# Performance work log

Measured on AMD Instinct MI355X. Metric: run time of the kernel, lower is better.

Reference implementation:

```python
import jax, jax.numpy as jnp
import numpy as np

NUM_EXPERTS = 8
IN_FEATURES = 1024
HIDDEN_FEATURES = 4096
OUT_FEATURES = 1024
TOKENS = 8192


def setup_inputs() -> dict:
    key = jax.random.key(0)
    k_x, k_idx, k_w1, k_w2, k_b1, k_b2 = jax.random.split(key, 6)
    x = jax.random.normal(k_x, (TOKENS, IN_FEATURES), dtype=jnp.float32)
    indices_s = jax.random.randint(k_idx, (TOKENS,), 0, NUM_EXPERTS, dtype=jnp.int64)
    # learned parameters (torch uses torch.rand; scaled for numeric sanity)
    weight1 = jax.random.normal(k_w1, (NUM_EXPERTS, IN_FEATURES, HIDDEN_FEATURES), dtype=jnp.float32) * 0.02
    weight2 = jax.random.normal(k_w2, (NUM_EXPERTS, HIDDEN_FEATURES, OUT_FEATURES), dtype=jnp.float32) * 0.02
    bias1 = jax.random.normal(k_b1, (NUM_EXPERTS, HIDDEN_FEATURES), dtype=jnp.float32) * 0.02
    bias2 = jax.random.normal(k_b2, (NUM_EXPERTS, IN_FEATURES), dtype=jnp.float32) * 0.02
    return {"x": x, "indices_s": indices_s, "weight1": weight1, "weight2": weight2, "bias1": bias1, "bias2": bias2}


def reference(x, indices_s, weight1, weight2, bias1, bias2):
    # Per-token expert MLP. Rather than gathering full weight matrices per
    # token (weight[indices_s] -> [T, in, hid], huge), loop over the small
    # fixed expert set and mask-combine. Math identical to the torch module.
    T = x.shape[0]
    num_experts = weight1.shape[0]
    out = jnp.zeros((T, weight2.shape[2]), dtype=x.dtype)
    for e in range(num_experts):
        mask = (indices_s == e)[:, None]  # [T, 1]
        h = jax.nn.gelu(x @ weight1[e] + bias1[e], approximate=False)  # [T, hid]
        y = h @ weight2[e] + bias2[e]  # [T, out]
        out = out + jnp.where(mask, y, jnp.zeros((), dtype=x.dtype))
    # original returns shape [T, 1, out] (x was unsqueezed)
    return out[:, None, :]
```

## Files before the change

kernel.cpp:

```cpp
#include <hip/hip_runtime.h>
#include <hip/hip_bf16.h>
#include <math.h>

#define TOKENS 8192
#define IN_F   1024
#define HID_F  4096
#define OUT_F  1024
#define NEXP   8
#define TSLOTS 72

typedef __attribute__((ext_vector_type(8))) short bf16x8;
typedef __attribute__((ext_vector_type(4))) float f32x4;
typedef __attribute__((ext_vector_type(8))) unsigned short u16x8;

__device__ __forceinline__ unsigned short f2bf(float f) {
    unsigned int u = __float_as_uint(f);
    u += 0x7fffu + ((u >> 16) & 1u);
    return (unsigned short)(u >> 16);
}

__device__ __forceinline__ void gload_lds16(const unsigned short* g, unsigned char* lds) {
    __builtin_amdgcn_global_load_lds(
        (const __attribute__((address_space(1))) void*)g,
        (__attribute__((address_space(3))) void*)lds, 16, 0, 0);
}

__global__ void sort_kernel(const int* __restrict__ idx, int* __restrict__ perm,
                            int* __restrict__ off, int* __restrict__ table) {
    __shared__ int cnt[NEXP];
    __shared__ int base[NEXP];
    const int tid = threadIdx.x, lane = tid & 63;
    if (tid < NEXP) cnt[tid] = 0;
    __syncthreads();
    for (int i = tid; i < TOKENS; i += 1024) {
        int e = idx[i];
#pragma unroll
        for (int ex = 0; ex < NEXP; ++ex) {
            unsigned long long m = __ballot(e == ex);
            if (lane == 0 && m) atomicAdd(&cnt[ex], __popcll(m));
        }
    }
    __syncthreads();
    if (tid == 0) {
        int s = 0;
        for (int e = 0; e < NEXP; ++e) { off[e] = s; base[e] = s; s += cnt[e]; }
        off[NEXP] = s;
        int t = 0;
        for (int e = 0; e < NEXP; ++e)
            for (int m0 = off[e]; m0 < off[e + 1]; m0 += 128)
                table[t++] = (e << 13) | m0;
        for (; t < TSLOTS; ++t) table[t] = -1;
    }
    __syncthreads();
    for (int i = tid; i < TOKENS; i += 1024) {
        int e = idx[i];
#pragma unroll
        for (int ex = 0; ex < NEXP; ++ex) {
            unsigned long long m = __ballot(e == ex);
            if (e == ex) {
                int lead = (int)__ffsll((long long)m) - 1;
                int pos = 0;
                if (lane == lead) pos = atomicAdd(&base[ex], __popcll(m));
                pos = __shfl(pos, lead);
                pos += __popcll(m & ((1ULL << lane) - 1ULL));
                perm[pos] = i;
            }
        }
    }
}

__global__ void gather_x(const float* __restrict__ x, const int* __restrict__ perm,
                         unsigned short* __restrict__ xg) {
    const int row = blockIdx.x, t = threadIdx.x;
    const int src = perm[row];
    float4 v = *(const float4*)(x + (size_t)src * IN_F + t * 4);
    unsigned long long pk =
        (unsigned long long)f2bf(v.x) |
        ((unsigned long long)f2bf(v.y) << 16) |
        ((unsigned long long)f2bf(v.z) << 32) |
        ((unsigned long long)f2bf(v.w) << 48);
    *(unsigned long long*)(xg + (size_t)row * IN_F + t * 4) = pk;
}

__global__ void transp(const float* __restrict__ in, unsigned short* __restrict__ out,
                       int R, int C) {
    __shared__ unsigned short T[64 * 65];
    const int e = blockIdx.z;
    const int r0 = blockIdx.y * 64, c0 = blockIdx.x * 64;
    const int tid = threadIdx.x;
    const int rr = tid >> 4, cc = tid & 15;
    const float* ip = in + ((size_t)e * R + r0) * C + c0;
#pragma unroll
    for (int p = 0; p < 4; ++p) {
        int r = p * 16 + rr;
        float4 v = *(const float4*)(ip + (size_t)r * C + cc * 4);
        T[(cc * 4 + 0) * 65 + r] = f2bf(v.x);
        T[(cc * 4 + 1) * 65 + r] = f2bf(v.y);
        T[(cc * 4 + 2) * 65 + r] = f2bf(v.z);
        T[(cc * 4 + 3) * 65 + r] = f2bf(v.w);
    }
    __syncthreads();
    unsigned short* op = out + ((size_t)e * C + c0) * R + r0;
    const int c = tid >> 2, ch = tid & 3;
    u16x8 a, b;
#pragma unroll
    for (int i = 0; i < 8; ++i) a[i] = T[c * 65 + ch * 16 + i];
#pragma unroll
    for (int i = 0; i < 8; ++i) b[i] = T[c * 65 + ch * 16 + 8 + i];
    *(u16x8*)(op + (size_t)c * R + ch * 16) = a;
    *(u16x8*)(op + (size_t)c * R + ch * 16 + 8) = b;
}

template<int K, int ND, bool GELU>
__launch_bounds__(256, 2)
__global__ void moe_gemm(const unsigned short* __restrict__ A,
                         const unsigned short* __restrict__ W,
                         const float* __restrict__ bias,
                         const int* __restrict__ perm,
                         const int* __restrict__ off,
                         const int* __restrict__ table,
                         void* __restrict__ outp) {
    const int nwg = (ND / 128) * TSLOTS;
    const int chunk = nwg >> 3;
    const int bid = blockIdx.x;
    const int logical = (bid & 7) * chunk + (bid >> 3);
    const int nt = logical / TSLOTS;
    const int t  = logical - nt * TSLOTS;
    const int te = table[t];
    if (te < 0) return;
    const int e  = te >> 13;
    const int m0 = te & 8191;
    const int sege = off[e + 1];
    const int n0 = nt * 128;

    __shared__ __align__(16) unsigned char As[16384];
    __shared__ __align__(16) unsigned char Bs[16384];

    const int tid = threadIdx.x;
    const int wid = tid >> 6, lane = tid & 63;
    const int wm = (wid >> 1) * 64, wn = (wid & 1) * 64;
    const int lr = lane & 15, hk = lane >> 4;

    const unsigned short* We = W + (size_t)e * ND * K + (size_t)n0 * K;

    const int srow   = lane >> 3;
    const int schunk = (lane & 7) ^ srow;

    f32x4 acc[4][4];
#pragma unroll
    for (int i = 0; i < 4; ++i)
#pragma unroll
        for (int j = 0; j < 4; ++j) acc[i][j] = (f32x4){0.f, 0.f, 0.f, 0.f};

    for (int k0 = 0; k0 < K; k0 += 64) {
        __syncthreads();
#pragma unroll
        for (int j = 0; j < 4; ++j) {
            int rt = (wid * 4 + j) * 8 + srow;
            int ga = m0 + rt; if (ga > TOKENS - 1) ga = TOKENS - 1;
            gload_lds16(A  + (size_t)ga * K + k0 + schunk * 8, As + (wid * 4 + j) * 1024);
            gload_lds16(We + (size_t)rt * K + k0 + schunk * 8, Bs + (wid * 4 + j) * 1024);
        }
        __syncthreads();
#pragma unroll
        for (int kk = 0; kk < 2; ++kk) {
            bf16x8 a[4], b[4];
#pragma unroll
            for (int m = 0; m < 4; ++m) {
                int row = wm + m * 16 + lr;
                a[m] = *(const bf16x8*)(As + row * 128 + (((kk * 4 + hk) ^ (lr & 7)) * 16));
            }
#pragma unroll
            for (int n = 0; n < 4; ++n) {
                int row = wn + n * 16 + lr;
                b[n] = *(const bf16x8*)(Bs + row * 128 + (((kk * 4 + hk) ^ (lr & 7)) * 16));
            }
#pragma unroll
            for (int m = 0; m < 4; ++m)
#pragma unroll
                for (int n = 0; n < 4; ++n)
                    acc[m][n] = __builtin_amdgcn_mfma_f32_16x16x32_bf16(a[m], b[n], acc[m][n], 0, 0, 0);
        }
    }

    const float* be = bias + (size_t)e * ND + n0;
#pragma unroll
    for (int m = 0; m < 4; ++m) {
#pragma unroll
        for (int r = 0; r < 4; ++r) {
            int row = wm + m * 16 + hk * 4 + r;
            int grow = m0 + row;
            if (grow >= sege) continue;
            if constexpr (GELU) {
                unsigned short* h = (unsigned short*)outp;
                size_t base = (size_t)grow * ND + n0;
#pragma unroll
                for (int n = 0; n < 4; ++n) {
                    int col = wn + n * 16 + lr;
                    float v = acc[m][n][r] + be[col];
                    float u = v * (0.7978845608f + 0.0356774081f * v * v);
                    float g = v / (1.0f + __expf(-2.0f * u));
                    h[base + col] = f2bf(g);
                }
            } else {
                float* out = (float*)outp;
                int tok = perm[grow];
                size_t base = (size_t)tok * ND + n0;
#pragma unroll
                for (int n = 0; n < 4; ++n) {
                    int col = wn + n * 16 + lr;
                    out[base + col] = acc[m][n][r] + be[col];
                }
            }
        }
    }
}

extern "C" void kernel_launch(void* const* d_in, const int* in_sizes, int n_in,
                              void* d_out, int out_size, void* d_ws, size_t ws_size,
                              hipStream_t stream) {
    const float* x   = (const float*)d_in[0];
    const int*   idx = (const int*)d_in[1];
    const float* w1  = (const float*)d_in[2];
    const float* w2  = (const float*)d_in[3];
    const float* b1  = (const float*)d_in[4];
    const float* b2  = (const float*)d_in[5];
    float* out = (float*)d_out;

    int* perm  = (int*)d_ws;
    int* off   = perm + TOKENS;
    int* table = off + 16;
    unsigned short* xg = (unsigned short*)((char*)d_ws + 65536);
    unsigned short* h  = xg + (size_t)TOKENS * IN_F;
    unsigned short* wt = h + (size_t)TOKENS * HID_F;

    hipLaunchKernelGGL(sort_kernel, dim3(1), dim3(1024), 0, stream, idx, perm, off, table);
    hipLaunchKernelGGL(gather_x, dim3(TOKENS), dim3(256), 0, stream, x, perm, xg);

    hipLaunchKernelGGL(transp, dim3(HID_F / 64, IN_F / 64, NEXP), dim3(256), 0, stream,
                       w1, wt, IN_F, HID_F);
    hipLaunchKernelGGL((moe_gemm<IN_F, HID_F, true>), dim3((HID_F / 128) * TSLOTS), dim3(256),
                       0, stream, xg, wt, b1, perm, off, table, (void*)h);

    hipLaunchKernelGGL(transp, dim3(OUT_F / 64, HID_F / 64, NEXP), dim3(256), 0, stream,
                       w2, wt, HID_F, OUT_F);
    hipLaunchKernelGGL((moe_gemm<HID_F, OUT_F, false>), dim3((OUT_F / 128) * TSLOTS), dim3(256),
                       0, stream, h, wt, b2, perm, off, table, (void*)out);
}
```

Measured before the change: 351.1 us.

## Pipeline MoE GEMM with 4-stage LDS ring buffer and async global loads

Replaces the single-buffered k-loop (two barriers per 64-wide k step) with a 4-deep ring of 32-wide k stages in 64 KB of LDS. Loads are issued three stages ahead and gated with explicit vmcnt waits, so there is one barrier per stage. The LDS swizzle changes to suit the 64-byte rows, and the MFMA block is raised in priority with setprio. The goal is to hide global-to-LDS load latency behind compute, at the cost of 64 KB of LDS per block, which may limit occupancy to 2 blocks per CU or below.

```diff
diff --git a/kernel.cpp b/kernel.cpp
--- a/kernel.cpp
+++ b/kernel.cpp
@@ -113,13 +113,13 @@
 
 template<int K, int ND, bool GELU>
 __launch_bounds__(256, 2)
-__global__ void moe_gemm(const unsigned short* __restrict__ A,
-                         const unsigned short* __restrict__ W,
-                         const float* __restrict__ bias,
-                         const int* __restrict__ perm,
-                         const int* __restrict__ off,
-                         const int* __restrict__ table,
-                         void* __restrict__ outp) {
+__global__ void moe_gemm_pipe(const unsigned short* __restrict__ A,
+                              const unsigned short* __restrict__ W,
+                              const float* __restrict__ bias,
+                              const int* __restrict__ perm,
+                              const int* __restrict__ off,
+                              const int* __restrict__ table,
+                              void* __restrict__ outp) {
     const int nwg = (ND / 128) * TSLOTS;
     const int chunk = nwg >> 3;
     const int bid = blockIdx.x;
@@ -133,8 +133,7 @@
     const int sege = off[e + 1];
     const int n0 = nt * 128;
 
-    __shared__ __align__(16) unsigned char As[16384];
-    __shared__ __align__(16) unsigned char Bs[16384];
+    __shared__ __align__(16) unsigned char L[65536];
 
     const int tid = threadIdx.x;
     const int wid = tid >> 6, lane = tid & 63;
@@ -143,8 +142,27 @@
 
     const unsigned short* We = W + (size_t)e * ND * K + (size_t)n0 * K;
 
-    const int srow   = lane >> 3;
-    const int schunk = (lane & 7) ^ srow;
+    const int id0 = tid, id1 = tid + 256;
+    const int ar0 = id0 >> 2, ac0 = (id0 & 3) ^ ((ar0 >> 1) & 3);
+    const int ar1 = id1 >> 2, ac1 = (id1 & 3) ^ ((ar1 >> 1) & 3);
+    int ga0 = m0 + ar0; if (ga0 > TOKENS - 1) ga0 = TOKENS - 1;
+    int ga1 = m0 + ar1; if (ga1 > TOKENS - 1) ga1 = TOKENS - 1;
+    const unsigned short* sA0 = A + (size_t)ga0 * K + ac0 * 8;
+    const unsigned short* sA1 = A + (size_t)ga1 * K + ac1 * 8;
+    const unsigned short* sB0 = We + (size_t)ar0 * K + ac0 * 8;
+    const unsigned short* sB1 = We + (size_t)ar1 * K + ac1 * 8;
+    const int du = wid * 1024;
+
+    constexpr int NS = K / 32;
+
+    auto stage = [&](int s) {
+        unsigned char* base = L + (s & 3) * 16384;
+        const int ko = s * 32;
+        gload_lds16(sA0 + ko, base + du);
+        gload_lds16(sA1 + ko, base + 4096 + du);
+        gload_lds16(sB0 + ko, base + 8192 + du);
+        gload_lds16(sB1 + ko, base + 12288 + du);
+    };
 
     f32x4 acc[4][4];
 #pragma unroll
@@ -152,35 +170,36 @@
 #pragma unroll
         for (int j = 0; j < 4; ++j) acc[i][j] = (f32x4){0.f, 0.f, 0.f, 0.f};
 
-    for (int k0 = 0; k0 < K; k0 += 64) {
-        __syncthreads();
-#pragma unroll
-        for (int j = 0; j < 4; ++j) {
-            int rt = (wid * 4 + j) * 8 + srow;
-            int ga = m0 + rt; if (ga > TOKENS - 1) ga = TOKENS - 1;
-            gload_lds16(A  + (size_t)ga * K + k0 + schunk * 8, As + (wid * 4 + j) * 1024);
-            gload_lds16(We + (size_t)rt * K + k0 + schunk * 8, Bs + (wid * 4 + j) * 1024);
-        }
-        __syncthreads();
-#pragma unroll
-        for (int kk = 0; kk < 2; ++kk) {
-            bf16x8 a[4], b[4];
-#pragma unroll
-            for (int m = 0; m < 4; ++m) {
-                int row = wm + m * 16 + lr;
-                a[m] = *(const bf16x8*)(As + row * 128 + (((kk * 4 + hk) ^ (lr & 7)) * 16));
-            }
-#pragma unroll
-            for (int n = 0; n < 4; ++n) {
-                int row = wn + n * 16 + lr;
-                b[n] = *(const bf16x8*)(Bs + row * 128 + (((kk * 4 + hk) ^ (lr & 7)) * 16));
-            }
-#pragma unroll
-            for (int m = 0; m < 4; ++m)
-#pragma unroll
-                for (int n = 0; n < 4; ++n)
-                    acc[m][n] = __builtin_amdgcn_mfma_f32_16x16x32_bf16(a[m], b[n], acc[m][n], 0, 0, 0);
-        }
+    stage(0); stage(1); stage(2);
+
+    for (int s = 0; s < NS; ++s) {
+        const int rem = NS - 1 - s;
+        if (rem >= 2)      asm volatile("s_waitcnt vmcnt(8)" ::: "memory");
+        else if (rem == 1) asm volatile("s_waitcnt vmcnt(4)" ::: "memory");
+        else               asm volatile("s_waitcnt vmcnt(0)" ::: "memory");
+        __builtin_amdgcn_s_barrier();
+        __builtin_amdgcn_sched_barrier(0);
+        if (s + 3 < NS) stage(s + 3);
+
+        const unsigned char* base = L + (s & 3) * 16384;
+        bf16x8 a[4], b[4];
+#pragma unroll
+        for (int m = 0; m < 4; ++m) {
+            int row = wm + m * 16 + lr;
+            a[m] = *(const bf16x8*)(base + row * 64 + ((hk ^ ((row >> 1) & 3)) << 4));
+        }
+#pragma unroll
+        for (int n = 0; n < 4; ++n) {
+            int row = wn + n * 16 + lr;
+            b[n] = *(const bf16x8*)(base + 8192 + row * 64 + ((hk ^ ((row >> 1) & 3)) << 4));
+        }
+        __builtin_amdgcn_s_setprio(1);
+#pragma unroll
+        for (int m = 0; m < 4; ++m)
+#pragma unroll
+            for (int n = 0; n < 4; ++n)
+                acc[m][n] = __builtin_amdgcn_mfma_f32_16x16x32_bf16(a[m], b[n], acc[m][n], 0, 0, 0);
+        __builtin_amdgcn_s_setprio(0);
     }
 
     const float* be = bias + (size_t)e * ND + n0;
@@ -239,11 +258,11 @@
 
     hipLaunchKernelGGL(transp, dim3(HID_F / 64, IN_F / 64, NEXP), dim3(256), 0, stream,
                        w1, wt, IN_F, HID_F);
-    hipLaunchKernelGGL((moe_gemm<IN_F, HID_F, true>), dim3((HID_F / 128) * TSLOTS), dim3(256),
+    hipLaunchKernelGGL((moe_gemm_pipe<IN_F, HID_F, true>), dim3((HID_F / 128) * TSLOTS), dim3(256),
                        0, stream, xg, wt, b1, perm, off, table, (void*)h);
 
     hipLaunchKernelGGL(transp, dim3(OUT_F / 64, HID_F / 64, NEXP), dim3(256), 0, stream,
                        w2, wt, HID_F, OUT_F);
-    hipLaunchKernelGGL((moe_gemm<HID_F, OUT_F, false>), dim3((OUT_F / 128) * TSLOTS), dim3(256),
+    hipLaunchKernelGGL((moe_gemm_pipe<HID_F, OUT_F, false>), dim3((OUT_F / 128) * TSLOTS), dim3(256),
                        0, stream, h, wt, b2, perm, off, table, (void*)out);
 }
```

Result: slower. 367.6 us (+4.7%).

## Use 256x256 MoE GEMM tiles with double-buffered LDS and interleaved prefetch

Applied to the files above, without the earlier changes.

Replaces the 128x128, 256-thread grouped GEMM with a 256x256 tile kernel using 512 threads and 128KB of double-buffered LDS. Token slots are now 256 rows, so TSLOTS drops to 40. The next K-tile is staged in four pieces interleaved with MFMA blocks, and s_setprio is raised around the MFMA bursts to overlap loads with compute. This increases operand reuse per LDS load and cuts global traffic. In exchange it gives far fewer workgroups, notably only 160 for the second GEMM on a 256-CU part, and higher register pressure.

```diff
diff --git a/kernel.cpp b/kernel.cpp
--- a/kernel.cpp
+++ b/kernel.cpp
@@ -7,7 +7,7 @@
 #define HID_F  4096
 #define OUT_F  1024
 #define NEXP   8
-#define TSLOTS 72
+#define TSLOTS 40
 
 typedef __attribute__((ext_vector_type(8))) short bf16x8;
 typedef __attribute__((ext_vector_type(4))) float f32x4;
@@ -47,7 +47,7 @@
         off[NEXP] = s;
         int t = 0;
         for (int e = 0; e < NEXP; ++e)
-            for (int m0 = off[e]; m0 < off[e + 1]; m0 += 128)
+            for (int m0 = off[e]; m0 < off[e + 1]; m0 += 256)
                 table[t++] = (e << 13) | m0;
         for (; t < TSLOTS; ++t) table[t] = -1;
     }
@@ -112,83 +112,141 @@
 }
 
 template<int K, int ND, bool GELU>
-__launch_bounds__(256, 2)
-__global__ void moe_gemm(const unsigned short* __restrict__ A,
-                         const unsigned short* __restrict__ W,
-                         const float* __restrict__ bias,
-                         const int* __restrict__ perm,
-                         const int* __restrict__ off,
-                         const int* __restrict__ table,
-                         void* __restrict__ outp) {
-    const int nwg = (ND / 128) * TSLOTS;
+__launch_bounds__(512, 2)
+__global__ void moe_gemm256(const unsigned short* __restrict__ A,
+                            const unsigned short* __restrict__ W,
+                            const float* __restrict__ bias,
+                            const int* __restrict__ perm,
+                            const int* __restrict__ off,
+                            const int* __restrict__ table,
+                            void* __restrict__ outp) {
+    const int nwg = (ND / 256) * TSLOTS;
     const int chunk = nwg >> 3;
-    const int bid = blockIdx.x;
-    const int logical = (bid & 7) * chunk + (bid >> 3);
+    const int logical = ((int)blockIdx.x & 7) * chunk + ((int)blockIdx.x >> 3);
     const int nt = logical / TSLOTS;
-    const int t  = logical - nt * TSLOTS;
-    const int te = table[t];
+    const int t0 = logical - nt * TSLOTS;
+    const int te = table[t0];
     if (te < 0) return;
     const int e  = te >> 13;
     const int m0 = te & 8191;
     const int sege = off[e + 1];
-    const int n0 = nt * 128;
-
-    __shared__ __align__(16) unsigned char As[16384];
-    __shared__ __align__(16) unsigned char Bs[16384];
+    const int n0 = nt * 256;
+
+    __shared__ __align__(16) unsigned char L[131072];
 
     const int tid = threadIdx.x;
     const int wid = tid >> 6, lane = tid & 63;
-    const int wm = (wid >> 1) * 64, wn = (wid & 1) * 64;
+    const int wr = wid >> 2, wc = wid & 3;
     const int lr = lane & 15, hk = lane >> 4;
 
     const unsigned short* We = W + (size_t)e * ND * K + (size_t)n0 * K;
 
-    const int srow   = lane >> 3;
-    const int schunk = (lane & 7) ^ srow;
-
-    f32x4 acc[4][4];
-#pragma unroll
-    for (int i = 0; i < 4; ++i)
+    const int srow8 = lane >> 3;
+    const int sch   = (lane & 7) ^ srow8;
+    const unsigned short* aSrc[4];
+    const unsigned short* wSrc[4];
+#pragma unroll
+    for (int cc = 0; cc < 4; ++cc) {
+        int rt = cc * 64 + wid * 8 + srow8;
+        int ga = m0 + rt; if (ga > TOKENS - 1) ga = TOKENS - 1;
+        aSrc[cc] = A  + (size_t)ga * K + sch * 8;
+        wSrc[cc] = We + (size_t)rt * K + sch * 8;
+    }
+    const int dstBase = wid * 1024;
+
+    constexpr int NT = K / 64;
+
+    auto stageH = [&](int tile, int h) {
+        const int buf = (tile & 1) * 65536;
+        const int op  = (h >> 1) * 32768;
+        const int c0_ = (h & 1) * 2;
+        const int ko  = tile * 64;
+#pragma unroll
+        for (int j = 0; j < 2; ++j) {
+            int cc = c0_ + j;
+            const unsigned short* s = (h < 2) ? (aSrc[cc] + ko) : (wSrc[cc] + ko);
+            gload_lds16(s, L + buf + op + cc * 8192 + dstBase);
+        }
+    };
+
+    f32x4 acc[8][4];
+#pragma unroll
+    for (int i = 0; i < 8; ++i)
 #pragma unroll
         for (int j = 0; j < 4; ++j) acc[i][j] = (f32x4){0.f, 0.f, 0.f, 0.f};
 
-    for (int k0 = 0; k0 < K; k0 += 64) {
-        __syncthreads();
-#pragma unroll
-        for (int j = 0; j < 4; ++j) {
-            int rt = (wid * 4 + j) * 8 + srow;
-            int ga = m0 + rt; if (ga > TOKENS - 1) ga = TOKENS - 1;
-            gload_lds16(A  + (size_t)ga * K + k0 + schunk * 8, As + (wid * 4 + j) * 1024);
-            gload_lds16(We + (size_t)rt * K + k0 + schunk * 8, Bs + (wid * 4 + j) * 1024);
-        }
-        __syncthreads();
-#pragma unroll
-        for (int kk = 0; kk < 2; ++kk) {
-            bf16x8 a[4], b[4];
-#pragma unroll
-            for (int m = 0; m < 4; ++m) {
-                int row = wm + m * 16 + lr;
-                a[m] = *(const bf16x8*)(As + row * 128 + (((kk * 4 + hk) ^ (lr & 7)) * 16));
-            }
-#pragma unroll
-            for (int n = 0; n < 4; ++n) {
-                int row = wn + n * 16 + lr;
-                b[n] = *(const bf16x8*)(Bs + row * 128 + (((kk * 4 + hk) ^ (lr & 7)) * 16));
-            }
-#pragma unroll
-            for (int m = 0; m < 4; ++m)
-#pragma unroll
-                for (int n = 0; n < 4; ++n)
-                    acc[m][n] = __builtin_amdgcn_mfma_f32_16x16x32_bf16(a[m], b[n], acc[m][n], 0, 0, 0);
-        }
+#pragma unroll
+    for (int h = 0; h < 4; ++h) stageH(0, h);
+
+    const int xorc = (lr & 7) << 4;
+
+    for (int t = 0; t < NT; ++t) {
+        __builtin_amdgcn_s_barrier();
+        if (t + 1 < NT) {
+            stageH(t + 1, 0);
+            asm volatile("s_waitcnt vmcnt(2)" ::: "memory");
+        } else {
+            asm volatile("s_waitcnt vmcnt(0)" ::: "memory");
+        }
+        __builtin_amdgcn_s_barrier();
+        __builtin_amdgcn_sched_barrier(0);
+
+        const unsigned char* rb = L + (t & 1) * 65536;
+
+        bf16x8 b[4][2];
+#pragma unroll
+        for (int n = 0; n < 4; ++n) {
+            int row = wc * 64 + n * 16 + lr;
+#pragma unroll
+            for (int kk = 0; kk < 2; ++kk)
+                b[n][kk] = *(const bf16x8*)(rb + 32768 + row * 128 + ((((kk * 4 + hk) << 4) ^ xorc)));
+        }
+
+        bf16x8 a[4][2];
+#pragma unroll
+        for (int m = 0; m < 4; ++m) {
+            int row = wr * 128 + m * 16 + lr;
+#pragma unroll
+            for (int kk = 0; kk < 2; ++kk)
+                a[m][kk] = *(const bf16x8*)(rb + row * 128 + ((((kk * 4 + hk) << 4) ^ xorc)));
+        }
+        if (t + 1 < NT) stageH(t + 1, 1);
+        __builtin_amdgcn_s_setprio(1);
+#pragma unroll
+        for (int m = 0; m < 4; ++m)
+#pragma unroll
+            for (int n = 0; n < 4; ++n)
+#pragma unroll
+                for (int kk = 0; kk < 2; ++kk)
+                    acc[m][n] = __builtin_amdgcn_mfma_f32_16x16x32_bf16(a[m][kk], b[n][kk], acc[m][n], 0, 0, 0);
+        __builtin_amdgcn_s_setprio(0);
+
+#pragma unroll
+        for (int m = 0; m < 4; ++m) {
+            int row = wr * 128 + 64 + m * 16 + lr;
+#pragma unroll
+            for (int kk = 0; kk < 2; ++kk)
+                a[m][kk] = *(const bf16x8*)(rb + row * 128 + ((((kk * 4 + hk) << 4) ^ xorc)));
+        }
+        if (t + 1 < NT) stageH(t + 1, 2);
+        __builtin_amdgcn_s_setprio(1);
+#pragma unroll
+        for (int m = 0; m < 4; ++m)
+#pragma unroll
+            for (int n = 0; n < 4; ++n)
+#pragma unroll
+                for (int kk = 0; kk < 2; ++kk)
+                    acc[4 + m][n] = __builtin_amdgcn_mfma_f32_16x16x32_bf16(a[m][kk], b[n][kk], acc[4 + m][n], 0, 0, 0);
+        __builtin_amdgcn_s_setprio(0);
+        if (t + 1 < NT) stageH(t + 1, 3);
     }
 
     const float* be = bias + (size_t)e * ND + n0;
 #pragma unroll
-    for (int m = 0; m < 4; ++m) {
+    for (int m = 0; m < 8; ++m) {
 #pragma unroll
         for (int r = 0; r < 4; ++r) {
-            int row = wm + m * 16 + hk * 4 + r;
+            int row = wr * 128 + m * 16 + hk * 4 + r;
             int grow = m0 + row;
             if (grow >= sege) continue;
             if constexpr (GELU) {
@@ -196,7 +254,7 @@
                 size_t base = (size_t)grow * ND + n0;
 #pragma unroll
                 for (int n = 0; n < 4; ++n) {
-                    int col = wn + n * 16 + lr;
+                    int col = wc * 64 + n * 16 + lr;
                     float v = acc[m][n][r] + be[col];
                     float u = v * (0.7978845608f + 0.0356774081f * v * v);
                     float g = v / (1.0f + __expf(-2.0f * u));
@@ -208,7 +266,7 @@
                 size_t base = (size_t)tok * ND + n0;
 #pragma unroll
                 for (int n = 0; n < 4; ++n) {
-                    int col = wn + n * 16 + lr;
+                    int col = wc * 64 + n * 16 + lr;
                     out[base + col] = acc[m][n][r] + be[col];
                 }
             }
@@ -239,11 +297,11 @@
 
     hipLaunchKernelGGL(transp, dim3(HID_F / 64, IN_F / 64, NEXP), dim3(256), 0, stream,
                        w1, wt, IN_F, HID_F);
-    hipLaunchKernelGGL((moe_gemm<IN_F, HID_F, true>), dim3((HID_F / 128) * TSLOTS), dim3(256),
+    hipLaunchKernelGGL((moe_gemm256<IN_F, HID_F, true>), dim3((HID_F / 256) * TSLOTS), dim3(512),
                        0, stream, xg, wt, b1, perm, off, table, (void*)h);
 
     hipLaunchKernelGGL(transp, dim3(OUT_F / 64, HID_F / 64, NEXP), dim3(256), 0, stream,
                        w2, wt, HID_F, OUT_F);
-    hipLaunchKernelGGL((moe_gemm<HID_F, OUT_F, false>), dim3((OUT_F / 128) * TSLOTS), dim3(256),
+    hipLaunchKernelGGL((moe_gemm256<HID_F, OUT_F, false>), dim3((OUT_F / 256) * TSLOTS), dim3(512),
                        0, stream, h, wt, b2, perm, off, table, (void*)out);
 }
```

Result: faster. 341.7 us (-2.7%).
